# Kernel tuning notes

Hardware: AMD Instinct MI355X
Metric: run time of the kernel (lower is better)

## Reference

```python
import jax, jax.numpy as jnp
import numpy as np

B, A, RF, F = 4096, 128, 128, 128  # batch, max_atom, res_n_features, n_features


def setup_inputs() -> dict:
    key = jax.random.key(0)
    k1, k2, k3, k4 = jax.random.split(key, 4)
    node_features = jax.random.normal(k1, (B, A, F), dtype=jnp.float32)
    residual_features = jax.random.normal(k2, (B, A, RF), dtype=jnp.float32)
    # Glorot-style init for the residual transform weight
    scale = jnp.sqrt(6.0 / (RF + F)).astype(jnp.float32)
    w = jax.random.uniform(k3, (RF, F), dtype=jnp.float32, minval=-scale, maxval=scale)
    # mol_slice[g] = [n_atoms_g, n_features]; atom counts vary per graph (ragged)
    atoms = jax.random.randint(k4, (B,), 1, A + 1, dtype=jnp.int64)
    mol_slice = jnp.stack([atoms, jnp.full((B,), F, dtype=jnp.int64)], axis=1)
    return {"node_features": node_features, "residual_features": residual_features,
            "w": w, "mol_slice": mol_slice}


def reference(node_features, residual_features, w, mol_slice):
    # Original: per-graph slice to [M_g, F], x_res @ w + x, pad back to max_atom,
    # then relu. Equivalent masked batched form: rows >= M_g become zeros.
    M = mol_slice[:, 0]  # [B] atom counts
    row_mask = (jnp.arange(A)[None, :] < M[:, None])[:, :, None]  # [B, A, 1]
    y = jnp.einsum('bar,rf->baf', residual_features, w) + node_features  # [B, A, F]
    return jnp.where(row_mask, jax.nn.relu(y), jnp.zeros((), dtype=y.dtype))
```

## Files before the change

### kernel.cpp

```cpp
#include <hip/hip_runtime.h>


typedef __bf16 bf16x8 __attribute__((ext_vector_type(8)));
typedef float f32x4 __attribute__((ext_vector_type(4)));

static_assert(sizeof(bf16x8) == 16, "bf16x8 must be 16B");
static_assert(sizeof(f32x4) == 16, "f32x4 must be 16B");

__global__ __launch_bounds__(256) void wT_kernel(const float* __restrict__ w,
                                                 __bf16* __restrict__ wT) {
    int i = blockIdx.x * 256 + threadIdx.x;
    int f = i >> 7;
    int r = i & 127;
    wT[i] = (__bf16)w[r * 128 + f];
}

__global__ __launch_bounds__(256, 4) void blockend_kernel(
    const float* __restrict__ node,
    const float* __restrict__ resid,
    const __bf16* __restrict__ wT,
    const int*   __restrict__ mol,
    float*       __restrict__ out)
{
    const int bb   = blockIdx.x;
    const int b    = bb >> 1;
    const int t    = threadIdx.x;
    const int wave = t >> 6;
    const int lane = t & 63;
    const int quad = lane >> 4;
    const int m16  = lane & 15;

    const int M      = mol[2 * b];
    const int a_base = (bb & 1) * 64 + wave * 16;

    const size_t base = (size_t)b * (128 * 128);
    float* outW = out + base + (size_t)a_base * 128;

    if (M <= a_base) {
        f32x4 z = {0.f, 0.f, 0.f, 0.f};
#pragma unroll
        for (int it = 0; it < 8; ++it)
            __builtin_nontemporal_store(z, (f32x4*)outW + it * 64 + lane);
        return;
    }

    const bool active = (a_base + m16) < M;
    const int  rrow   = active ? m16 : 0;

    const float* residW = resid + base + (size_t)a_base * 128;
    const float* nodeW  = node  + base + (size_t)a_base * 128;

    bf16x8 rfrag[4];
#pragma unroll
    for (int kk = 0; kk < 4; ++kk) {
        const float* ap = residW + rrow * 128 + kk * 32 + quad * 8;
        f32x4 lo = *(const f32x4*)ap;
        f32x4 hi = *(const f32x4*)(ap + 4);
        bf16x8 v;
        v[0] = (__bf16)lo[0]; v[1] = (__bf16)lo[1];
        v[2] = (__bf16)lo[2]; v[3] = (__bf16)lo[3];
        v[4] = (__bf16)hi[0]; v[5] = (__bf16)hi[1];
        v[6] = (__bf16)hi[2]; v[7] = (__bf16)hi[3];
        rfrag[kk] = v;
    }

#pragma unroll
    for (int ft = 0; ft < 8; ++ft) {
        f32x4 acc = {0.f, 0.f, 0.f, 0.f};
#pragma unroll
        for (int kk = 0; kk < 4; ++kk) {
            bf16x8 wfrag = *(const bf16x8*)(wT + (ft * 16 + m16) * 128 + kk * 32 + quad * 8);
            acc = __builtin_amdgcn_mfma_f32_16x16x32_bf16(wfrag, rfrag[kk], acc, 0, 0, 0);
        }
        const int offs = ft * 16 + quad * 4;
        f32x4 nd = *(const f32x4*)(nodeW + rrow * 128 + offs);
        f32x4 v;
#pragma unroll
        for (int i = 0; i < 4; ++i) {
            float x = acc[i] + nd[i];
            v[i] = (active && x > 0.f) ? x : 0.f;
        }
        __builtin_nontemporal_store(v, (f32x4*)(outW + m16 * 128 + offs));
    }
}

extern "C" void kernel_launch(void* const* d_in, const int* in_sizes, int n_in,
                              void* d_out, int out_size, void* d_ws, size_t ws_size,
                              hipStream_t stream) {
    const float* node  = (const float*)d_in[0];
    const float* resid = (const float*)d_in[1];
    const float* w     = (const float*)d_in[2];
    const int*   mol   = (const int*)d_in[3];
    float*       out   = (float*)d_out;
    __bf16*      wT    = (__bf16*)d_ws;

    wT_kernel<<<64, 256, 0, stream>>>(w, wT);
    blockend_kernel<<<8192, 256, 0, stream>>>(node, resid, wT, mol, out);
}
```

Measured before the change: 650.1 us.

## Persistent kernel with double-buffered global-to-LDS DMA and LDS-resident swizzled weights

Replaces the one-block-per-half-graph launch with a persistent grid of 256 blocks of 3 waves. Each wave loops over 16-row tiles and prefetches the next tile's residual and node rows into LDS with global_load_lds while it computes the current one. The weight matrix is pre-swizzled into bf16 and kept in LDS to avoid bank conflicts and repeated global loads. This is meant to hide memory latency and raise bandwidth use. In exchange it needs 128KB of LDS per block at one block per CU, hand-tuned vmcnt waits, and plain stores in place of nontemporal ones.

```diff
diff --git a/kernel.cpp b/kernel.cpp
--- a/kernel.cpp
+++ b/kernel.cpp
@@ -7,80 +7,157 @@
 static_assert(sizeof(bf16x8) == 16, "bf16x8 must be 16B");
 static_assert(sizeof(f32x4) == 16, "f32x4 must be 16B");
 
+#define NT 32768
+#define NW 768
+#define LDS_TOTAL 131072
+
 __global__ __launch_bounds__(256) void wT_kernel(const float* __restrict__ w,
-                                                 __bf16* __restrict__ wT) {
-    int i = blockIdx.x * 256 + threadIdx.x;
-    int f = i >> 7;
-    int r = i & 127;
-    wT[i] = (__bf16)w[r * 128 + f];
+                                                 __bf16* __restrict__ wTs) {
+    int i  = blockIdx.x * 256 + threadIdx.x;
+    int f  = i >> 7;
+    int k  = i & 127;
+    int cu = k >> 3;
+    int j  = k & 7;
+    int r  = ((cu ^ (f & 7)) << 3) | j;
+    wTs[i] = (__bf16)w[r * 128 + f];
 }
 
-__global__ __launch_bounds__(256, 4) void blockend_kernel(
+__device__ __forceinline__ void issue_dma_region(const char* gmol, char* slotRegion,
+                                                 int aBase, int M, int lrow2, int lcol) {
+#pragma unroll
+    for (int i = 0; i < 8; ++i) {
+        const int row  = 2 * i + lrow2;
+        const int grow = min(aBase + row, M - 1);
+        const int gb   = grow * 512 + ((lcol ^ (row & 7)) << 4);
+        auto src = (const __attribute__((address_space(1))) unsigned int*)(gmol + gb);
+        auto dst = (__attribute__((address_space(3))) unsigned int*)(slotRegion + i * 1024);
+        __builtin_amdgcn_global_load_lds(src, dst, 16, 0, 0);
+    }
+}
+
+__global__ __launch_bounds__(192, 1) void blockend_kernel(
     const float* __restrict__ node,
     const float* __restrict__ resid,
-    const __bf16* __restrict__ wT,
+    const __bf16* __restrict__ wTs,
     const int*   __restrict__ mol,
     float*       __restrict__ out)
 {
-    const int bb   = blockIdx.x;
-    const int b    = bb >> 1;
-    const int t    = threadIdx.x;
-    const int wave = t >> 6;
-    const int lane = t & 63;
-    const int quad = lane >> 4;
-    const int m16  = lane & 15;
+    extern __shared__ __attribute__((aligned(16))) char smem[];
 
-    const int M      = mol[2 * b];
-    const int a_base = (bb & 1) * 64 + wave * 16;
+    const int t     = threadIdx.x;
+    const int lane  = t & 63;
+    const int quad  = lane >> 4;
+    const int m16   = lane & 15;
+    const int lrow2 = lane >> 5;
+    const int lcol  = lane & 31;
+    const int wv    = __builtin_amdgcn_readfirstlane(t >> 6);
 
-    const size_t base = (size_t)b * (128 * 128);
-    float* outW = out + base + (size_t)a_base * 128;
+    {
+        const bf16x8* srcw = (const bf16x8*)wTs;
+        for (int u = t; u < 2048; u += 192)
+            *(bf16x8*)(smem + u * 16) = srcw[u];
+    }
+    __syncthreads();
 
-    if (M <= a_base) {
-        f32x4 z = {0.f, 0.f, 0.f, 0.f};
-#pragma unroll
-        for (int it = 0; it < 8; ++it)
-            __builtin_nontemporal_store(z, (f32x4*)outW + it * 64 + lane);
-        return;
+    char* slot0 = smem + 32768 + wv * 32768;
+    char* slot1 = slot0 + 16384;
+
+    const int wid = blockIdx.x * 3 + wv;
+
+    int tau   = wid;
+    int b0    = __builtin_amdgcn_readfirstlane(tau >> 3);
+    int M_cur = mol[2 * b0];
+    int b1    = __builtin_amdgcn_readfirstlane((tau + NW) >> 3);
+    int M_next = mol[2 * b1];
+
+    {
+        const char* rm = (const char*)resid + (size_t)b0 * 65536;
+        const char* nm = (const char*)node  + (size_t)b0 * 65536;
+        const int aB = (tau & 7) * 16;
+        issue_dma_region(rm, slot0,        aB, M_cur, lrow2, lcol);
+        issue_dma_region(nm, slot0 + 8192, aB, M_cur, lrow2, lcol);
     }
 
-    const bool active = (a_base + m16) < M;
-    const int  rrow   = active ? m16 : 0;
+    int p = 0;
+    bool first = true;
 
-    const float* residW = resid + base + (size_t)a_base * 128;
-    const float* nodeW  = node  + base + (size_t)a_base * 128;
+    for (; tau < NT; tau += NW) {
+        {
+            const int tn = min(tau + NW, NT - 1);
+            const int bn = tn >> 3;
+            const char* rm = (const char*)resid + (size_t)bn * 65536;
+            const char* nm = (const char*)node  + (size_t)bn * 65536;
+            char* s = p ? slot0 : slot1;
+            const int aB = (tn & 7) * 16;
+            issue_dma_region(rm, s,        aB, M_next, lrow2, lcol);
+            issue_dma_region(nm, s + 8192, aB, M_next, lrow2, lcol);
+        }
+        const int bn2 = __builtin_amdgcn_readfirstlane(min(tau + 2 * NW, NT - 1) >> 3);
+        const int M_next2 = mol[2 * bn2];
 
-    bf16x8 rfrag[4];
+        __builtin_amdgcn_sched_barrier(0);
+        if (first) { asm volatile("s_waitcnt vmcnt(16)" ::: "memory"); first = false; }
+        else       { asm volatile("s_waitcnt vmcnt(24)" ::: "memory"); }
+        __builtin_amdgcn_sched_barrier(0);
+
+        {
+            const int b     = tau >> 3;
+            const int aBase = (tau & 7) * 16;
+            float* outW = out + (size_t)b * 16384 + (size_t)aBase * 128;
+            const char* S = p ? slot1 : slot0;
+
+            if (aBase < M_cur) {
+                const int x = m16 & 7;
+                bf16x8 rfrag[4];
 #pragma unroll
-    for (int kk = 0; kk < 4; ++kk) {
-        const float* ap = residW + rrow * 128 + kk * 32 + quad * 8;
-        f32x4 lo = *(const f32x4*)ap;
-        f32x4 hi = *(const f32x4*)(ap + 4);
-        bf16x8 v;
-        v[0] = (__bf16)lo[0]; v[1] = (__bf16)lo[1];
-        v[2] = (__bf16)lo[2]; v[3] = (__bf16)lo[3];
-        v[4] = (__bf16)hi[0]; v[5] = (__bf16)hi[1];
-        v[6] = (__bf16)hi[2]; v[7] = (__bf16)hi[3];
-        rfrag[kk] = v;
-    }
-
+                for (int kk = 0; kk < 4; ++kk) {
+                    const int u0 = kk * 8 + quad * 2;
+                    f32x4 lo = *(const f32x4*)(S + m16 * 512 + (((u0    ) ^ x) << 4));
+                    f32x4 hi = *(const f32x4*)(S + m16 * 512 + (((u0 + 1) ^ x) << 4));
+                    bf16x8 v;
+                    v[0] = (__bf16)lo[0]; v[1] = (__bf16)lo[1];
+                    v[2] = (__bf16)lo[2]; v[3] = (__bf16)lo[3];
+                    v[4] = (__bf16)hi[0]; v[5] = (__bf16)hi[1];
+                    v[6] = (__bf16)hi[2]; v[7] = (__bf16)hi[3];
+                    rfrag[kk] = v;
+                }
+                f32x4 acc[8];
 #pragma unroll
-    for (int ft = 0; ft < 8; ++ft) {
-        f32x4 acc = {0.f, 0.f, 0.f, 0.f};
+                for (int ft = 0; ft < 8; ++ft) acc[ft] = (f32x4){0.f, 0.f, 0.f, 0.f};
 #pragma unroll
-        for (int kk = 0; kk < 4; ++kk) {
-            bf16x8 wfrag = *(const bf16x8*)(wT + (ft * 16 + m16) * 128 + kk * 32 + quad * 8);
-            acc = __builtin_amdgcn_mfma_f32_16x16x32_bf16(wfrag, rfrag[kk], acc, 0, 0, 0);
+                for (int ft = 0; ft < 8; ++ft)
+#pragma unroll
+                    for (int kk = 0; kk < 4; ++kk) {
+                        bf16x8 wfrag = *(const bf16x8*)(smem + ft * 4096 + m16 * 256
+                                            + ((((kk << 2) | quad) ^ x) << 4));
+                        acc[ft] = __builtin_amdgcn_mfma_f32_16x16x32_bf16(
+                            wfrag, rfrag[kk], acc[ft], 0, 0, 0);
+                    }
+                const bool act = (aBase + m16) < M_cur;
+#pragma unroll
+                for (int ft = 0; ft < 8; ++ft) {
+                    const int un = ft * 4 + quad;
+                    f32x4 nd = *(const f32x4*)(S + 8192 + m16 * 512 + ((un ^ x) << 4));
+                    f32x4 v;
+#pragma unroll
+                    for (int i = 0; i < 4; ++i) {
+                        float xx = acc[ft][i] + nd[i];
+                        v[i] = (act && xx > 0.f) ? xx : 0.f;
+                    }
+                    *(f32x4*)(outW + m16 * 128 + ft * 16 + quad * 4) = v;
+                }
+            } else {
+                f32x4 z = {0.f, 0.f, 0.f, 0.f};
+                f32x4* pp = (f32x4*)outW;
+#pragma unroll
+                for (int it = 0; it < 8; ++it)
+                    pp[it * 64 + lane] = z;
+            }
         }
-        const int offs = ft * 16 + quad * 4;
-        f32x4 nd = *(const f32x4*)(nodeW + rrow * 128 + offs);
-        f32x4 v;
-#pragma unroll
-        for (int i = 0; i < 4; ++i) {
-            float x = acc[i] + nd[i];
-            v[i] = (active && x > 0.f) ? x : 0.f;
-        }
-        __builtin_nontemporal_store(v, (f32x4*)(outW + m16 * 128 + offs));
+        __builtin_amdgcn_sched_barrier(0);
+        p ^= 1;
+        M_cur  = M_next;
+        M_next = M_next2;
     }
 }
 
@@ -92,8 +169,15 @@
     const float* w     = (const float*)d_in[2];
     const int*   mol   = (const int*)d_in[3];
     float*       out   = (float*)d_out;
-    __bf16*      wT    = (__bf16*)d_ws;
+    __bf16*      wTs   = (__bf16*)d_ws;
 
-    wT_kernel<<<64, 256, 0, stream>>>(w, wT);
-    blockend_kernel<<<8192, 256, 0, stream>>>(node, resid, wT, mol, out);
+    static bool attr_set = false;
+    if (!attr_set) {
+        hipFuncSetAttribute(reinterpret_cast<const void*>(blockend_kernel),
+                            hipFuncAttributeMaxDynamicSharedMemorySize, LDS_TOTAL);
+        attr_set = true;
+    }
+
+    wT_kernel<<<64, 256, 0, stream>>>(w, wTs);
+    blockend_kernel<<<256, 192, LDS_TOTAL, stream>>>(node, resid, wTs, mol, out);
 }
```

Result: faster. 560.2 us (-13.8%).
